# Kernel tuning notes

Hardware: AMD Instinct MI355X
Metric: run time of the kernel (lower is better)

Reference implementation:

```python
import jax, jax.numpy as jnp
import numpy as np

B, S, D_MODEL = 1, 2048, 2048
H, KVH = 16, 4
HD = D_MODEL // H          # 128
N_REP = H // KVH           # 4 (GQA)
WINDOW = 1024              # window_size=(WINDOW-1, 0): self + 1023 past tokens
CLIP = 8.0
THETA = 500000.0
EPS = 1e-6
SCALE = 1.0 / (HD ** 0.5)


def rms_norm(x, w):
    # per-head RMSNorm over last dim (head_dim)
    var = jnp.mean(jnp.square(x), axis=-1, keepdims=True)
    return x * jax.lax.rsqrt(var + EPS) * w


def rope_tables():
    inv_freq = 1.0 / (THETA ** (jnp.arange(0, HD, 2, dtype=jnp.float32) / HD))
    pos = jnp.arange(S, dtype=jnp.float32)
    freqs = pos[:, None] * inv_freq[None, :]          # [S, HD/2]
    emb = jnp.concatenate([freqs, freqs], axis=-1)    # [S, HD]
    return jnp.cos(emb), jnp.sin(emb)


def rotate_half(x):
    x1, x2 = x[..., : HD // 2], x[..., HD // 2 :]
    return jnp.concatenate([-x2, x1], axis=-1)


def apply_rope(x, cos, sin):
    # x: [B, S, h, HD]; cos/sin: [S, HD]
    return x * cos[None, :, None, :] + rotate_half(x) * sin[None, :, None, :]


def setup_inputs() -> dict:
    key = jax.random.key(0)
    ks = jax.random.split(key, 7)
    w = lambda k, shape: jax.random.normal(k, shape, jnp.float32) * 0.02
    return {
        "x": jax.random.normal(ks[0], (B, S, D_MODEL), jnp.float32),
        "w_q": w(ks[1], (D_MODEL, D_MODEL)),
        "w_k": w(ks[2], (KVH * HD, D_MODEL)),
        "w_v": w(ks[3], (KVH * HD, D_MODEL)),
        "w_out": w(ks[4], (D_MODEL, D_MODEL)),
        "q_norm_w": jnp.ones((HD,), jnp.float32),
        "k_norm_w": jnp.ones((HD,), jnp.float32),
        "sinks": jax.random.normal(ks[5], (H,), jnp.float32),
    }


def reference(x, w_q, w_k, w_v, w_out, q_norm_w, k_norm_w, sinks):
    # fused QKV projection + clip
    q = jnp.clip(x @ w_q.T, -CLIP, CLIP).reshape(B, S, H, HD)
    k = jnp.clip(x @ w_k.T, -CLIP, CLIP).reshape(B, S, KVH, HD)
    v = jnp.clip(x @ w_v.T, -CLIP, CLIP).reshape(B, S, KVH, HD)

    # per-head qk RMSNorm, then RoPE
    q = rms_norm(q, q_norm_w)
    k = rms_norm(k, k_norm_w)
    cos, sin = rope_tables()
    q = apply_rope(q, cos, sin)
    k = apply_rope(k, cos, sin)

    # GQA: repeat_interleave kv heads
    k = jnp.repeat(k, N_REP, axis=2)  # [B, S, H, HD]
    v = jnp.repeat(v, N_REP, axis=2)

    # sliding-window causal attention with a learned per-head sink logit
    logits = jnp.einsum("bqhd,bkhd->bhqk", q, k) * SCALE  # [B, H, S, S]
    qi = jnp.arange(S)[:, None]
    ki = jnp.arange(S)[None, :]
    mask = (ki <= qi) & (ki > qi - WINDOW)                # causal + window
    logits = jnp.where(mask[None, None, :, :], logits, -jnp.inf)

    # sink token: always-visible extra logit sinks[h] with zero value vector
    sink_col = jnp.broadcast_to(sinks[None, :, None, None], (B, H, S, 1))
    full = jnp.concatenate([logits, sink_col], axis=-1)   # [B, H, S, S+1]
    probs = jax.nn.softmax(full, axis=-1)

    att = jnp.einsum("bhqk,bkhd->bqhd", probs[..., :S], v)  # sink value is 0
    return att.reshape(B, S, D_MODEL) @ w_out.T
```

## Files before the change

kernel.cpp:

```cpp
#include <hip/hip_runtime.h>
#include <hip/hip_bf16.h>
#include <math.h>

#define S_LEN 2048
#define DMODEL 2048
#define NH 16
#define NKVH 4
#define HDIM 128
#define WINDOW 1024

typedef __bf16 bf16;
typedef __bf16 bf16x8 __attribute__((ext_vector_type(8)));
typedef __bf16 bf16x4 __attribute__((ext_vector_type(4)));
typedef float floatx4 __attribute__((ext_vector_type(4)));

static __device__ __forceinline__ bf16x8 load_bf8(const bf16* p) {
    return *reinterpret_cast<const bf16x8*>(p);
}

static __device__ __forceinline__ void async16(const bf16* g, bf16* l) {
    __builtin_amdgcn_global_load_lds(
        (const __attribute__((address_space(1))) void*)g,
        (__attribute__((address_space(3))) void*)l, 16, 0, 0);
}

__global__ __launch_bounds__(256) void convert_kernel(
    const float* __restrict__ x, const float* __restrict__ wq,
    const float* __restrict__ wk, const float* __restrict__ wv,
    bf16* __restrict__ xb, bf16* __restrict__ wqb, bf16* __restrict__ wkb,
    bf16* __restrict__ wvb) {
    for (int i = blockIdx.x * blockDim.x + threadIdx.x; i < 2621440;
         i += gridDim.x * blockDim.x) {
        const float* src; bf16* dst; int off;
        if      (i < 1048576) { src = x;  dst = xb;  off = i; }
        else if (i < 2097152) { src = wq; dst = wqb; off = i - 1048576; }
        else if (i < 2359296) { src = wk; dst = wkb; off = i - 2097152; }
        else                  { src = wv; dst = wvb; off = i - 2359296; }
        float4 v = reinterpret_cast<const float4*>(src)[off];
        union { bf16 b[4]; ushort4 u; } t;
        t.b[0] = (bf16)v.x; t.b[1] = (bf16)v.y;
        t.b[2] = (bf16)v.z; t.b[3] = (bf16)v.w;
        reinterpret_cast<ushort4*>(dst)[off] = t.u;
    }
}

#define GEMM_BODY()                                                            \
    __shared__ __align__(16) bf16 smem[2 * (64 + 128) * 64];        \
    int tid = threadIdx.x;                                                     \
    int lane = tid & 63, wid = tid >> 6;                                       \
    int l15 = lane & 15, quad = lane >> 4;                                     \
    int rlocal = lane >> 3;                                                    \
    int scol = ((lane & 7) ^ rlocal) * 8;                                      \
    const bf16* gA = A + (size_t)(m0 + wid * 16 + rlocal) * K + scol;          \
    const bf16* gB = B + (size_t)(n0 + wid * 32 + rlocal) * K + scol;          \
    int ldsOfA = (wid * 16) * 64;                                               \
    int ldsOfB = (wid * 32) * 64;                                               \
    floatx4 acc[2][4];                                                         \
    _Pragma("unroll") for (int mi = 0; mi < 2; ++mi)                           \
        _Pragma("unroll") for (int ni = 0; ni < 4; ++ni)                       \
            acc[mi][ni] = floatx4{0.f, 0.f, 0.f, 0.f};                         \
    int mb = (wid & 1) * 32, nb = (wid >> 1) * 64;                             \
    _Pragma("unroll") for (int j = 0; j < 2; ++j)                              \
        async16(gA + (size_t)(j * 8) * K, smem + ldsOfA + j * 512);            \
    _Pragma("unroll") for (int j = 0; j < 4; ++j)                              \
        async16(gB + (size_t)(j * 8) * K, smem + 8192 + ldsOfB + j * 512);     \
    int buf = 0;                                                               \
    for (int k0 = 0; k0 < K; k0 += 64) {                                       \
        __syncthreads();                                                       \
        if (k0 + 64 < K) {                                                     \
            int nof = buf ^ 1;                                                 \
            _Pragma("unroll") for (int j = 0; j < 2; ++j)                      \
                async16(gA + (size_t)(j * 8) * K + k0 + 64,                    \
                        smem + nof * 4096 + ldsOfA + j * 512);                 \
            _Pragma("unroll") for (int j = 0; j < 4; ++j)                      \
                async16(gB + (size_t)(j * 8) * K + k0 + 64,                    \
                        smem + 8192 + nof * 8192 + ldsOfB + j * 512);          \
        }                                                                      \
        const bf16* sA = smem + buf * 4096;                                    \
        const bf16* sB = smem + 8192 + buf * 8192;                             \
        _Pragma("unroll") for (int kc = 0; kc < 2; ++kc) {                     \
            bf16x8 af[2], bq[4];                                               \
            int ch = ((kc << 2) + quad) ^ (l15 & 7);                           \
            _Pragma("unroll") for (int i = 0; i < 2; ++i)                      \
                af[i] = load_bf8(sA + (mb + i * 16 + l15) * 64 + ch * 8);      \
            _Pragma("unroll") for (int i = 0; i < 4; ++i)                      \
                bq[i] = load_bf8(sB + (nb + i * 16 + l15) * 64 + ch * 8);      \
            _Pragma("unroll") for (int mi = 0; mi < 2; ++mi)                   \
                _Pragma("unroll") for (int ni = 0; ni < 4; ++ni)               \
                    acc[mi][ni] = __builtin_amdgcn_mfma_f32_16x16x32_bf16(     \
                        af[mi], bq[ni], acc[mi][ni], 0, 0, 0);                 \
        }                                                                      \
        buf ^= 1;                                                              \
    }

__global__ __launch_bounds__(256, 1) void gemm_qkv_fused(
    const bf16* __restrict__ A, const bf16* __restrict__ B,
    const float* __restrict__ qw, const float* __restrict__ kw,
    bf16* __restrict__ qb, bf16* __restrict__ kb, bf16* __restrict__ vtb) {
    const int K = 2048;
    int m0 = blockIdx.y * 128, n0 = blockIdx.x * 256;
    __shared__ __align__(16) bf16 smem[2 * 24576];
    int tid = threadIdx.x;
    int lane = tid & 63, wid = tid >> 6;
    int l15 = lane & 15, quad = lane >> 4;
    int rlocal = lane >> 3;
    int scol = ((lane & 7) ^ rlocal) * 8;
    const bf16* gA = A + (size_t)(m0 + wid * 32 + rlocal) * K + scol;
    const bf16* gB = B + (size_t)(n0 + wid * 64 + rlocal) * K + scol;
    int mb = (wid & 1) * 64, nb = (wid >> 1) * 128;

    floatx4 acc[4][8];
#pragma unroll
    for (int mi = 0; mi < 4; ++mi)
#pragma unroll
        for (int ni = 0; ni < 8; ++ni) acc[mi][ni] = floatx4{0.f, 0.f, 0.f, 0.f};

#pragma unroll
    for (int j = 0; j < 4; ++j)
        async16(gA + (size_t)(j * 8) * K, smem + (wid * 32 + j * 8) * 64);
#pragma unroll
    for (int j = 0; j < 8; ++j)
        async16(gB + (size_t)(j * 8) * K, smem + 8192 + (wid * 64 + j * 8) * 64);

    int buf = 0;
    for (int k0 = 0; k0 < K; k0 += 64) {
        __syncthreads();
        if (k0 + 64 < K) {
            bf16* nbase = smem + (buf ^ 1) * 24576;
#pragma unroll
            for (int j = 0; j < 4; ++j)
                async16(gA + (size_t)(j * 8) * K + k0 + 64,
                        nbase + (wid * 32 + j * 8) * 64);
#pragma unroll
            for (int j = 0; j < 8; ++j)
                async16(gB + (size_t)(j * 8) * K + k0 + 64,
                        nbase + 8192 + (wid * 64 + j * 8) * 64);
        }
        const bf16* sA = smem + buf * 24576;
        const bf16* sB = sA + 8192;
#pragma unroll
        for (int kc = 0; kc < 2; ++kc) {
            bf16x8 af[4], bq[8];
            int ch = ((kc << 2) + quad) ^ (l15 & 7);
#pragma unroll
            for (int i = 0; i < 4; ++i)
                af[i] = load_bf8(sA + (mb + i * 16 + l15) * 64 + ch * 8);
#pragma unroll
            for (int n = 0; n < 8; ++n)
                bq[n] = load_bf8(sB + (nb + n * 16 + l15) * 64 + ch * 8);
#pragma unroll
            for (int mi = 0; mi < 4; ++mi)
#pragma unroll
                for (int ni = 0; ni < 8; ++ni)
                    acc[mi][ni] = __builtin_amdgcn_mfma_f32_16x16x32_bf16(
                        af[mi], bq[ni], acc[mi][ni], 0, 0, 0);
        }
        buf ^= 1;
    }

#pragma unroll
    for (int mi = 0; mi < 4; ++mi)
#pragma unroll
        for (int ni = 0; ni < 8; ++ni)
#pragma unroll
            for (int r = 0; r < 4; ++r)
                acc[mi][ni][r] = fminf(fmaxf(acc[mi][ni][r], -8.0f), 8.0f);

    if (n0 >= 2560) {
#pragma unroll
        for (int mi = 0; mi < 4; ++mi)
#pragma unroll
            for (int ni = 0; ni < 8; ++ni)
#pragma unroll
                for (int r = 0; r < 4; ++r) {
                    int row = m0 + mb + mi * 16 + quad * 4 + r;
                    int n = n0 + nb + ni * 16 + l15;
                    vtb[(size_t)(n - 2560) * 2048 + row] = (bf16)acc[mi][ni][r];
                }
        return;
    }

    const float* nw = (n0 < 2048) ? qw : kw;
    float nwv[8];
#pragma unroll
    for (int ni = 0; ni < 8; ++ni) nwv[ni] = nw[(nb + ni * 16 + l15) & 127];
#pragma unroll
    for (int mi = 0; mi < 4; ++mi)
#pragma unroll
        for (int r = 0; r < 4; ++r) {
            float s = 0.f;
#pragma unroll
            for (int ni = 0; ni < 8; ++ni) s += acc[mi][ni][r] * acc[mi][ni][r];
#pragma unroll
            for (int o = 1; o < 16; o <<= 1) s += __shfl_xor(s, o, 64);
            float rinv = rsqrtf(s * (1.0f / 128.0f) + 1e-6f);
#pragma unroll
            for (int ni = 0; ni < 8; ++ni) acc[mi][ni][r] *= rinv * nwv[ni];
        }

    float invf[4];
#pragma unroll
    for (int ni = 0; ni < 4; ++ni) {
        int fi = ni * 16 + l15;
        invf[ni] = __expf((float)fi * (-13.122363377404328f / 64.0f));
    }
#pragma unroll
    for (int mi = 0; mi < 4; ++mi)
#pragma unroll
        for (int r = 0; r < 4; ++r) {
            int row = mb + mi * 16 + quad * 4 + r;
            int s = m0 + row;
            float pos = (float)s;
#pragma unroll
            for (int ni = 0; ni < 4; ++ni) {
                float ang = pos * invf[ni];
                float c = __cosf(ang), sn = __sinf(ang);
                float a = acc[mi][ni][r], b2 = acc[mi][ni + 4][r];
                float olo = a * c - b2 * sn;
                float ohi = b2 * c + a * sn;
                int nlo = n0 + nb + ni * 16 + l15;
                if (n0 < 2048) {
                    qb[(size_t)s * 2048 + nlo] = (bf16)olo;
                    qb[(size_t)s * 2048 + nlo + 64] = (bf16)ohi;
                } else {
                    kb[(size_t)s * 512 + (nlo - 2048)] = (bf16)olo;
                    kb[(size_t)s * 512 + (nlo - 2048) + 64] = (bf16)ohi;
                }
            }
        }
}

__global__ __launch_bounds__(256) void gemm_out(
    const bf16* __restrict__ A, const bf16* __restrict__ B,
    float* __restrict__ C) {
    const int K = 2048, N = 2048;
    int m0 = blockIdx.y * 64, n0 = blockIdx.x * 128;
    GEMM_BODY()
#pragma unroll
    for (int mi = 0; mi < 2; ++mi)
#pragma unroll
        for (int ni = 0; ni < 4; ++ni)
#pragma unroll
            for (int r = 0; r < 4; ++r) {
                int m = m0 + mb + mi * 16 + quad * 4 + r;
                int n = n0 + nb + ni * 16 + l15;
                C[(size_t)m * N + n] = acc[mi][ni][r];
            }
}

__global__ __launch_bounds__(256) void attn(
    const bf16* __restrict__ qb, const bf16* __restrict__ kb,
    const bf16* __restrict__ vtb, const float* __restrict__ sinks,
    const float* __restrict__ wo, bf16* __restrict__ wob,
    bf16* __restrict__ attb) {
    __shared__ __align__(16) bf16 sK[2][64 * 128];
    __shared__ __align__(16) bf16 sV[2][128 * 64];
    __shared__ __align__(16) bf16 sP[64 * 72];
    __shared__ float redu[64][4];
    int tid = threadIdx.x;
    int lane = tid & 63, wid = tid >> 6;
    int l15 = lane & 15, quad = lane >> 4;
    int h = blockIdx.y, kh = h >> 2;
    int bq0 = blockIdx.x * 64;

    {
        int bindex = blockIdx.y * gridDim.x + blockIdx.x;
        for (int i = bindex * 256 + tid; i < 1048576; i += 512 * 256) {
            float4 v = reinterpret_cast<const float4*>(wo)[i];
            union { bf16 b[4]; ushort4 u; } t2;
            t2.b[0] = (bf16)v.x; t2.b[1] = (bf16)v.y;
            t2.b[2] = (bf16)v.z; t2.b[3] = (bf16)v.w;
            reinterpret_cast<ushort4*>(wob)[i] = t2.u;
        }
    }

    bf16x8 qf[4][4];
#pragma unroll
    for (int ni = 0; ni < 4; ++ni) {
        const bf16* qrow = qb + (size_t)(bq0 + ni * 16 + l15) * 2048 + h * 128 + quad * 8;
#pragma unroll
        for (int kc = 0; kc < 4; ++kc) qf[ni][kc] = load_bf8(qrow + kc * 32);
    }

    floatx4 acc[4][2];
#pragma unroll
    for (int mi = 0; mi < 4; ++mi)
#pragma unroll
        for (int df = 0; df < 2; ++df) acc[mi][df] = floatx4{0.f, 0.f, 0.f, 0.f};
    float lpq[4];
#pragma unroll
    for (int ni = 0; ni < 4; ++ni) lpq[ni] = 0.f;

    int keyit = wid * 4 + (lane >> 4);
    int gcK = (lane & 15) ^ keyit;
    int dimit = wid * 8 + (lane >> 3);
    int gcV = (lane & 7) ^ ((lane >> 3) & 7);

    int tstart = bq0 - 1024; if (tstart < 0) tstart = 0;
    const bf16* kbase = kb + (size_t)kh * 128;
    const bf16* vbase = vtb + (size_t)kh * 128 * 2048;

#pragma unroll
    for (int r = 0; r < 4; ++r) {
        async16(kbase + (size_t)(tstart + r * 16 + keyit) * 512 + gcK * 8,
                sK[0] + (r * 16 + wid * 4) * 128);
        async16(vbase + (size_t)(r * 32 + dimit) * 2048 + tstart + gcV * 8,
                sV[0] + (r * 32 + wid * 8) * 64);
    }

    int buf = 0;
    for (int t = tstart; t <= bq0; t += 64) {
        __syncthreads();
        if (t + 64 <= bq0) {
#pragma unroll
            for (int r = 0; r < 4; ++r) {
                async16(kbase + (size_t)(t + 64 + r * 16 + keyit) * 512 + gcK * 8,
                        sK[buf ^ 1] + (r * 16 + wid * 4) * 128);
                async16(vbase + (size_t)(r * 32 + dimit) * 2048 + t + 64 + gcV * 8,
                        sV[buf ^ 1] + (r * 32 + wid * 8) * 64);
            }
        }
        floatx4 ST[4];
#pragma unroll
        for (int ni = 0; ni < 4; ++ni) ST[ni] = floatx4{0.f, 0.f, 0.f, 0.f};
#pragma unroll
        for (int kc = 0; kc < 4; ++kc) {
            int ch = (kc * 4 + quad) ^ l15;
            bf16x8 kf = load_bf8(sK[buf] + (wid * 16 + l15) * 128 + ch * 8);
#pragma unroll
            for (int ni = 0; ni < 4; ++ni)
                ST[ni] = __builtin_amdgcn_mfma_f32_16x16x32_bf16(kf, qf[ni][kc], ST[ni], 0, 0, 0);
        }
        int kbi = t + wid * 16 + quad * 4;
        bool fullt = (t <= bq0 - 64) && (t >= bq0 - 960);
        if (fullt) {
#pragma unroll
            for (int ni = 0; ni < 4; ++ni) {
                bf16x4 pv;
#pragma unroll
                for (int r = 0; r < 4; ++r) {
                    float e = __expf(ST[ni][r] * 0.08838834764831845f);
                    lpq[ni] += e;
                    pv[r] = (bf16)e;
                }
                *(bf16x4*)(sP + (ni * 16 + l15) * 72 + wid * 16 + quad * 4) = pv;
            }
        } else {
#pragma unroll
            for (int ni = 0; ni < 4; ++ni) {
                int qi = bq0 + ni * 16 + l15;
                bf16x4 pv;
#pragma unroll
                for (int r = 0; r < 4; ++r) {
                    int ki = kbi + r;
                    float v = ST[ni][r] * 0.08838834764831845f;
                    bool ok = (ki <= qi) && (ki > qi - WINDOW);
                    float e = ok ? __expf(v) : 0.0f;
                    lpq[ni] += e;
                    pv[r] = (bf16)e;
                }
                *(bf16x4*)(sP + (ni * 16 + l15) * 72 + wid * 16 + quad * 4) = pv;
            }
        }
        __syncthreads();
#pragma unroll
        for (int kc = 0; kc < 2; ++kc) {
            bf16x8 pf[4];
#pragma unroll
            for (int mi = 0; mi < 4; ++mi)
                pf[mi] = load_bf8(sP + (mi * 16 + l15) * 72 + kc * 32 + quad * 8);
#pragma unroll
            for (int df = 0; df < 2; ++df) {
                int dim = wid * 32 + df * 16 + l15;
                int ch = (kc * 4 + quad) ^ (l15 & 7);
                bf16x8 vf = load_bf8(sV[buf] + dim * 64 + ch * 8);
#pragma unroll
                for (int mi = 0; mi < 4; ++mi)
                    acc[mi][df] = __builtin_amdgcn_mfma_f32_16x16x32_bf16(pf[mi], vf, acc[mi][df], 0, 0, 0);
            }
        }
        buf ^= 1;
    }

#pragma unroll
    for (int ni = 0; ni < 4; ++ni) {
        float v = lpq[ni];
        v += __shfl_xor(v, 16, 64);
        v += __shfl_xor(v, 32, 64);
        if (quad == 0) redu[ni * 16 + l15][wid] = v;
    }
    __syncthreads();
    float sk = __expf(sinks[h]);
#pragma unroll
    for (int mi = 0; mi < 4; ++mi)
#pragma unroll
        for (int r = 0; r < 4; ++r) {
            int row = mi * 16 + quad * 4 + r;
            float rs = redu[row][0] + redu[row][1] + redu[row][2] + redu[row][3] + sk;
            float inv = 1.0f / rs;
#pragma unroll
            for (int df = 0; df < 2; ++df) {
                int dim = wid * 32 + df * 16 + l15;
                attb[(size_t)(bq0 + row) * 2048 + h * 128 + dim] =
                    (bf16)(acc[mi][df][r] * inv);
            }
        }
}

extern "C" void kernel_launch(void* const* d_in, const int* in_sizes, int n_in,
                              void* d_out, int out_size, void* d_ws, size_t ws_size,
                              hipStream_t stream) {
    const float* x      = (const float*)d_in[0];
    const float* w_q    = (const float*)d_in[1];
    const float* w_k    = (const float*)d_in[2];
    const float* w_v    = (const float*)d_in[3];
    const float* w_out  = (const float*)d_in[4];
    const float* q_norm = (const float*)d_in[5];
    const float* k_norm = (const float*)d_in[6];
    const float* sinks  = (const float*)d_in[7];

    char* ws = (char*)d_ws;
    const size_t MB = 1u << 20;
    bf16* xb   = (bf16*)(ws + 0 * MB);
    bf16* wqb  = (bf16*)(ws + 8 * MB);
    bf16* wkb  = (bf16*)(ws + 16 * MB);
    bf16* wvb  = (bf16*)(ws + 18 * MB);
    bf16* wob  = (bf16*)(ws + 20 * MB);
    bf16* qb   = (bf16*)(ws + 28 * MB);
    bf16* kb   = (bf16*)(ws + 36 * MB);
    bf16* vtb  = (bf16*)(ws + 38 * MB);
    bf16* attb = (bf16*)(ws + 40 * MB);
    bf16* wcomb = wqb;
    float* out = (float*)d_out;

    convert_kernel<<<2048, 256, 0, stream>>>(x, w_q, w_k, w_v,
                                             xb, wqb, wkb, wvb);
    gemm_qkv_fused<<<dim3(12, 16), 256, 0, stream>>>(xb, wcomb, q_norm, k_norm,
                                                     qb, kb, vtb);
    attn<<<dim3(32, 16), 256, 0, stream>>>(qb, kb, vtb, sinks, w_out, wob, attb);
    gemm_out<<<dim3(16, 32), 256, 0, stream>>>(attb, wob, out);
}
```

Before: 200.8 us.

## Fuse QKV weight fp32-to-bf16 conversion into the QKV GEMM tile loads

The weight conversion for w_q, w_k and w_v moves out of the standalone convert kernel and into the QKV GEMM. Each GEMM block now reads fp32 weight tiles into registers, converts them to bf16 after the MFMA work, and stores them to the next LDS buffer. This removes a full write and re-read of the bf16 weight copies in global memory. In exchange, every one of the 16 M-blocks reads the fp32 weights (twice the bytes of bf16), the async direct-to-LDS path is lost for B, and register pressure rises from the prefetched float4s.

```diff
diff --git a/kernel.cpp b/kernel.cpp
--- a/kernel.cpp
+++ b/kernel.cpp
@@ -25,22 +25,14 @@
 }
 
 __global__ __launch_bounds__(256) void convert_kernel(
-    const float* __restrict__ x, const float* __restrict__ wq,
-    const float* __restrict__ wk, const float* __restrict__ wv,
-    bf16* __restrict__ xb, bf16* __restrict__ wqb, bf16* __restrict__ wkb,
-    bf16* __restrict__ wvb) {
-    for (int i = blockIdx.x * blockDim.x + threadIdx.x; i < 2621440;
+    const float* __restrict__ x, bf16* __restrict__ xb) {
+    for (int i = blockIdx.x * blockDim.x + threadIdx.x; i < 1048576;
          i += gridDim.x * blockDim.x) {
-        const float* src; bf16* dst; int off;
-        if      (i < 1048576) { src = x;  dst = xb;  off = i; }
-        else if (i < 2097152) { src = wq; dst = wqb; off = i - 1048576; }
-        else if (i < 2359296) { src = wk; dst = wkb; off = i - 2097152; }
-        else                  { src = wv; dst = wvb; off = i - 2359296; }
-        float4 v = reinterpret_cast<const float4*>(src)[off];
+        float4 v = reinterpret_cast<const float4*>(x)[i];
         union { bf16 b[4]; ushort4 u; } t;
         t.b[0] = (bf16)v.x; t.b[1] = (bf16)v.y;
         t.b[2] = (bf16)v.z; t.b[3] = (bf16)v.w;
-        reinterpret_cast<ushort4*>(dst)[off] = t.u;
+        reinterpret_cast<ushort4*>(xb)[i] = t.u;
     }
 }
 
@@ -94,7 +86,8 @@
     }
 
 __global__ __launch_bounds__(256, 1) void gemm_qkv_fused(
-    const bf16* __restrict__ A, const bf16* __restrict__ B,
+    const bf16* __restrict__ A, const float* __restrict__ wq,
+    const float* __restrict__ wk, const float* __restrict__ wv,
     const float* __restrict__ qw, const float* __restrict__ kw,
     bf16* __restrict__ qb, bf16* __restrict__ kb, bf16* __restrict__ vtb) {
     const int K = 2048;
@@ -106,7 +99,11 @@
     int rlocal = lane >> 3;
     int scol = ((lane & 7) ^ rlocal) * 8;
     const bf16* gA = A + (size_t)(m0 + wid * 32 + rlocal) * K + scol;
-    const bf16* gB = B + (size_t)(n0 + wid * 64 + rlocal) * K + scol;
+    const float* Bsrc; int nb0;
+    if (n0 < 2048)      { Bsrc = wq; nb0 = n0; }
+    else if (n0 < 2560) { Bsrc = wk; nb0 = n0 - 2048; }
+    else                { Bsrc = wv; nb0 = n0 - 2560; }
+    const float* gBf = Bsrc + (size_t)(nb0 + wid * 64 + rlocal) * K + scol;
     int mb = (wid & 1) * 64, nb = (wid >> 1) * 128;
 
     floatx4 acc[4][8];
@@ -119,22 +116,36 @@
     for (int j = 0; j < 4; ++j)
         async16(gA + (size_t)(j * 8) * K, smem + (wid * 32 + j * 8) * 64);
 #pragma unroll
-    for (int j = 0; j < 8; ++j)
-        async16(gB + (size_t)(j * 8) * K, smem + 8192 + (wid * 64 + j * 8) * 64);
+    for (int j = 0; j < 8; ++j) {
+        const float* s = gBf + (size_t)(j * 8) * K;
+        float4 v0 = *reinterpret_cast<const float4*>(s);
+        float4 v1 = *reinterpret_cast<const float4*>(s + 4);
+        union { bf16 b[8]; bf16x8 v; } t;
+        t.b[0] = (bf16)v0.x; t.b[1] = (bf16)v0.y;
+        t.b[2] = (bf16)v0.z; t.b[3] = (bf16)v0.w;
+        t.b[4] = (bf16)v1.x; t.b[5] = (bf16)v1.y;
+        t.b[6] = (bf16)v1.z; t.b[7] = (bf16)v1.w;
+        *reinterpret_cast<bf16x8*>(
+            smem + 8192 + (wid * 64 + j * 8) * 64 + lane * 8) = t.v;
+    }
 
     int buf = 0;
     for (int k0 = 0; k0 < K; k0 += 64) {
         __syncthreads();
-        if (k0 + 64 < K) {
+        bool hasNext = (k0 + 64 < K);
+        float4 pre[8][2];
+        if (hasNext) {
             bf16* nbase = smem + (buf ^ 1) * 24576;
 #pragma unroll
             for (int j = 0; j < 4; ++j)
                 async16(gA + (size_t)(j * 8) * K + k0 + 64,
                         nbase + (wid * 32 + j * 8) * 64);
 #pragma unroll
-            for (int j = 0; j < 8; ++j)
-                async16(gB + (size_t)(j * 8) * K + k0 + 64,
-                        nbase + 8192 + (wid * 64 + j * 8) * 64);
+            for (int j = 0; j < 8; ++j) {
+                const float* s = gBf + (size_t)(j * 8) * K + k0 + 64;
+                pre[j][0] = *reinterpret_cast<const float4*>(s);
+                pre[j][1] = *reinterpret_cast<const float4*>(s + 4);
+            }
         }
         const bf16* sA = smem + buf * 24576;
         const bf16* sB = sA + 8192;
@@ -154,6 +165,19 @@
                 for (int ni = 0; ni < 8; ++ni)
                     acc[mi][ni] = __builtin_amdgcn_mfma_f32_16x16x32_bf16(
                         af[mi], bq[ni], acc[mi][ni], 0, 0, 0);
+        }
+        if (hasNext) {
+            bf16* nbase = smem + (buf ^ 1) * 24576;
+#pragma unroll
+            for (int j = 0; j < 8; ++j) {
+                union { bf16 b[8]; bf16x8 v; } t;
+                t.b[0] = (bf16)pre[j][0].x; t.b[1] = (bf16)pre[j][0].y;
+                t.b[2] = (bf16)pre[j][0].z; t.b[3] = (bf16)pre[j][0].w;
+                t.b[4] = (bf16)pre[j][1].x; t.b[5] = (bf16)pre[j][1].y;
+                t.b[6] = (bf16)pre[j][1].z; t.b[7] = (bf16)pre[j][1].w;
+                *reinterpret_cast<bf16x8*>(
+                    nbase + 8192 + (wid * 64 + j * 8) * 64 + lane * 8) = t.v;
+            }
         }
         buf ^= 1;
     }
@@ -422,20 +446,16 @@
     char* ws = (char*)d_ws;
     const size_t MB = 1u << 20;
     bf16* xb   = (bf16*)(ws + 0 * MB);
-    bf16* wqb  = (bf16*)(ws + 8 * MB);
-    bf16* wkb  = (bf16*)(ws + 16 * MB);
-    bf16* wvb  = (bf16*)(ws + 18 * MB);
     bf16* wob  = (bf16*)(ws + 20 * MB);
     bf16* qb   = (bf16*)(ws + 28 * MB);
     bf16* kb   = (bf16*)(ws + 36 * MB);
     bf16* vtb  = (bf16*)(ws + 38 * MB);
     bf16* attb = (bf16*)(ws + 40 * MB);
-    bf16* wcomb = wqb;
     float* out = (float*)d_out;
 
-    convert_kernel<<<2048, 256, 0, stream>>>(x, w_q, w_k, w_v,
-                                             xb, wqb, wkb, wvb);
-    gemm_qkv_fused<<<dim3(12, 16), 256, 0, stream>>>(xb, wcomb, q_norm, k_norm,
+    convert_kernel<<<2048, 256, 0, stream>>>(x, xb);
+    gemm_qkv_fused<<<dim3(12, 16), 256, 0, stream>>>(xb, w_q, w_k, w_v,
+                                                     q_norm, k_norm,
                                                      qb, kb, vtb);
     attn<<<dim3(32, 16), 256, 0, stream>>>(qb, kb, vtb, sinks, w_out, wob, attb);
     gemm_out<<<dim3(16, 32), 256, 0, stream>>>(attb, wob, out);
```

New measurement: 263.2 us. 1.31x slower.
